# Optimization experiments

Hardware: AMD Instinct MI355X
Metric: run time of the kernel (lower is better)

Reference implementation:

```python
import jax, jax.numpy as jnp
import numpy as np

B = 32768          # batch (replay-buffer minibatch)
OBS, ACT = 17, 6   # HalfCheetah-style dims
IN = OBS + ACT
H = 256            # hidden width hard-coded in the module
N = 10             # num_q_nets


def setup_inputs() -> dict:
    key = jax.random.key(0)
    ks = jax.random.split(key, 8)
    # PyTorch Linear default init: U(-1/sqrt(fan_in), 1/sqrt(fan_in)); scale randn similarly.
    s1, s2, s3 = 1.0 / np.sqrt(IN), 1.0 / np.sqrt(H), 1.0 / np.sqrt(H)
    return {
        "state": jax.random.normal(ks[0], (B, OBS), dtype=jnp.float32),
        "action": jax.random.uniform(ks[1], (B, ACT), dtype=jnp.float32, minval=-1.0, maxval=1.0),
        "W1": jax.random.normal(ks[2], (N, IN, H), dtype=jnp.float32) * s1,
        "b1": jax.random.normal(ks[3], (N, H), dtype=jnp.float32) * s1,
        "W2": jax.random.normal(ks[4], (N, H, H), dtype=jnp.float32) * s2,
        "b2": jax.random.normal(ks[5], (N, H), dtype=jnp.float32) * s2,
        "W3": jax.random.normal(ks[6], (N, H, 1), dtype=jnp.float32) * s3,
        "b3": jax.random.normal(ks[7], (N, 1), dtype=jnp.float32) * s3,
    }


def reference(state, action, W1, b1, W2, b2, W3, b3):
    # x: [B, OBS+ACT]
    x = jnp.concatenate([state, action], axis=1)
    # batched-over-ensemble GEMMs; n=ensemble member, b=batch
    h1 = jax.nn.relu(jnp.einsum("bi,nih->nbh", x, W1) + b1[:, None, :])   # [N,B,H]
    h2 = jax.nn.relu(jnp.einsum("nbh,nho->nbo", h1, W2) + b2[:, None, :])  # [N,B,H]
    out = jnp.einsum("nbh,nho->nbo", h2, W3) + b3[:, None, :]              # [N,B,1]
    return out
```

## Files before the change

### kernel.cpp

```cpp
#include <hip/hip_runtime.h>
#include <hip/hip_bf16.h>


typedef __attribute__((ext_vector_type(8))) short bf16x8;
typedef __attribute__((ext_vector_type(4))) float f32x4;

#define B_TOTAL 32768
#define NQ 10
#define HDIM 256
#define BT 64

#define XP_ELEMS  (B_TOTAL * 32)
#define W1P_ELEMS (NQ * 16 * 64 * 8)
#define W2P_ELEMS (NQ * 8 * 16 * 64 * 8)

__device__ __forceinline__ unsigned short f2bf(float f) {
  unsigned int u = __float_as_uint(f);
  u = u + 0x7FFFu + ((u >> 16) & 1u);
  return (unsigned short)(u >> 16);
}

__device__ __forceinline__ unsigned int pk2bf(float a, float b) {
  union { __hip_bfloat162 h; unsigned int u; } cv;
  cv.h = __float22bfloat162_rn(make_float2(a, b));
  return cv.u;
}

__global__ void pack_all_kernel(const float* __restrict__ state,
                                const float* __restrict__ action,
                                const float* __restrict__ W1,
                                const float* __restrict__ W2,
                                unsigned short* __restrict__ xp,
                                unsigned short* __restrict__ w1p,
                                unsigned short* __restrict__ w2p) {
  int t = blockIdx.x * 256 + threadIdx.x;
  const int NX  = B_TOTAL * 4;
  const int NW1 = NQ * 16 * 64;
  if (t < NX) {
    int b = t >> 2, seg = t & 3;
    unsigned short v[8];
    if (seg < 2) {
      const float* sp = state + (size_t)b * 17 + seg * 8;
#pragma unroll
      for (int j = 0; j < 8; j++) v[j] = f2bf(sp[j]);
    } else if (seg == 2) {
      v[0] = f2bf(state[(size_t)b * 17 + 16]);
#pragma unroll
      for (int j = 0; j < 6; j++) v[1 + j] = f2bf(action[(size_t)b * 6 + j]);
      v[7] = 0;
    } else {
#pragma unroll
      for (int j = 0; j < 8; j++) v[j] = 0;
    }
    *(uint4*)&xp[(size_t)t * 8] = *(const uint4*)v;
  } else if (t < NX + NW1) {
    int u = t - NX;
    int lane = u & 63, mt = (u >> 6) & 15, n = u >> 10;
    int m = lane & 15, q = lane >> 4;
    int outc = mt * 16 + m;
    unsigned short v[8];
#pragma unroll
    for (int j = 0; j < 8; j++) {
      int k = q * 8 + j;
      v[j] = (k < 23) ? f2bf(W1[(n * 23 + k) * 256 + outc]) : (unsigned short)0;
    }
    *(uint4*)&w1p[(size_t)u * 8] = *(const uint4*)v;
  } else {
    int u = t - NX - NW1;
    int lane = u & 63, mt = (u >> 6) & 15, kt = (u >> 10) & 7, n = u >> 13;
    int m = lane & 15, q = lane >> 4;
    int outc = mt * 16 + m;
    unsigned short v[8];
#pragma unroll
    for (int j = 0; j < 8; j++) {
      int h = kt * 32 + q * 8 + j;
      v[j] = f2bf(W2[((size_t)(n * 256 + h)) * 256 + outc]);
    }
    *(uint4*)&w2p[(size_t)u * 8] = *(const uint4*)v;
  }
}

__global__ __launch_bounds__(256, 4) void fused_ensemble_kernel(
    const unsigned short* __restrict__ xp,
    const unsigned short* __restrict__ w1p,
    const float* __restrict__ b1,
    const unsigned short* __restrict__ w2p,
    const float* __restrict__ b2,
    const float* __restrict__ W3,
    const float* __restrict__ b3,
    float* __restrict__ out) {
  __shared__ __align__(16) unsigned short hs[32 * BT * 8];
  __shared__ float red[4 * 64];

  const int tid = threadIdx.x;
  const int lane = tid & 63;
  const int w = tid >> 6;
  const int m = lane & 15;
  const int q = lane >> 4;

  const int n = blockIdx.x >> 9;
  const int row0 = (blockIdx.x & 511) * BT;

  f32x4 acc[4][4];

  {
    bf16x8 af[4], bfr[4];
#pragma unroll
    for (int nt = 0; nt < 4; nt++) {
      int col = row0 + nt * 16 + m;
      bfr[nt] = *(const bf16x8*)(xp + (size_t)col * 32 + q * 8);
    }
#pragma unroll
    for (int mt = 0; mt < 4; mt++)
      af[mt] = *(const bf16x8*)(w1p + (((size_t)n * 16 + w * 4 + mt) * 64 + lane) * 8);
#pragma unroll
    for (int mt = 0; mt < 4; mt++) {
      float4 bv = *(const float4*)&b1[n * HDIM + (w * 4 + mt) * 16 + q * 4];
      f32x4 bi = (f32x4){bv.x, bv.y, bv.z, bv.w};
#pragma unroll
      for (int nt = 0; nt < 4; nt++) acc[mt][nt] = bi;
    }
    __builtin_amdgcn_s_setprio(1);
#pragma unroll
    for (int nt = 0; nt < 4; nt++)
#pragma unroll
      for (int mt = 0; mt < 4; mt++)
        acc[mt][nt] = __builtin_amdgcn_mfma_f32_16x16x32_bf16(af[mt], bfr[nt], acc[mt][nt], 0, 0, 0);
    __builtin_amdgcn_s_setprio(0);
  }

#pragma unroll
  for (int mt = 0; mt < 4; mt++) {
    int kq = w * 8 + mt * 2 + (q >> 1);
    int joff = (q & 1) * 4;
#pragma unroll
    for (int nt = 0; nt < 4; nt++) {
      int col = nt * 16 + m;
      f32x4 a = acc[mt][nt];
      uint2 wv;
      wv.x = pk2bf(fmaxf(a[0], 0.f), fmaxf(a[1], 0.f));
      wv.y = pk2bf(fmaxf(a[2], 0.f), fmaxf(a[3], 0.f));
      *(uint2*)&hs[((size_t)kq * BT + col) * 8 + joff] = wv;
    }
  }
  __syncthreads();

  {
    const unsigned short* w2n = w2p + (size_t)n * (8 * 16 * 64 * 8);
    bf16x8 acur[4], anxt[4];
#pragma unroll
    for (int mt = 0; mt < 4; mt++)
      acur[mt] = *(const bf16x8*)(w2n + (((size_t)w * 4 + mt) * 64 + lane) * 8);
#pragma unroll
    for (int mt = 0; mt < 4; mt++) {
      float4 bv = *(const float4*)&b2[n * HDIM + (w * 4 + mt) * 16 + q * 4];
      f32x4 bi = (f32x4){bv.x, bv.y, bv.z, bv.w};
#pragma unroll
      for (int nt = 0; nt < 4; nt++) acc[mt][nt] = bi;
    }
#pragma unroll
    for (int kt = 0; kt < 8; kt++) {
      if (kt < 7) {
#pragma unroll
        for (int mt = 0; mt < 4; mt++)
          anxt[mt] = *(const bf16x8*)(w2n + (((size_t)(kt + 1) * 16 + w * 4 + mt) * 64 + lane) * 8);
      }
      bf16x8 bfr[4];
#pragma unroll
      for (int nt = 0; nt < 4; nt++)
        bfr[nt] = *(const bf16x8*)&hs[(((size_t)kt * 4 + q) * BT + nt * 16 + m) * 8];
      __builtin_amdgcn_s_setprio(1);
#pragma unroll
      for (int nt = 0; nt < 4; nt++)
#pragma unroll
        for (int mt = 0; mt < 4; mt++)
          acc[mt][nt] = __builtin_amdgcn_mfma_f32_16x16x32_bf16(acur[mt], bfr[nt], acc[mt][nt], 0, 0, 0);
      __builtin_amdgcn_s_setprio(0);
#pragma unroll
      for (int mt = 0; mt < 4; mt++) acur[mt] = anxt[mt];
    }
  }

  {
    float4 w3v[4];
#pragma unroll
    for (int mt = 0; mt < 4; mt++)
      w3v[mt] = *(const float4*)&W3[n * HDIM + (w * 4 + mt) * 16 + q * 4];
    float p[4];
#pragma unroll
    for (int nt = 0; nt < 4; nt++) {
      float s = 0.f;
#pragma unroll
      for (int mt = 0; mt < 4; mt++) {
        f32x4 a = acc[mt][nt];
        float4 wv = w3v[mt];
        s = fmaf(fmaxf(a[0], 0.f), wv.x, s);
        s = fmaf(fmaxf(a[1], 0.f), wv.y, s);
        s = fmaf(fmaxf(a[2], 0.f), wv.z, s);
        s = fmaf(fmaxf(a[3], 0.f), wv.w, s);
      }
      s += __shfl_xor(s, 16, 64);
      s += __shfl_xor(s, 32, 64);
      p[nt] = s;
    }
    if (q == 0) {
#pragma unroll
      for (int nt = 0; nt < 4; nt++) red[w * 64 + nt * 16 + m] = p[nt];
    }
    __syncthreads();
    if (tid < BT) {
      float s = b3[n];
#pragma unroll
      for (int c = 0; c < 4; c++) s += red[c * 64 + tid];
      out[(size_t)n * B_TOTAL + row0 + tid] = s;
    }
  }
}

extern "C" void kernel_launch(void* const* d_in, const int* in_sizes, int n_in,
                              void* d_out, int out_size, void* d_ws, size_t ws_size,
                              hipStream_t stream) {
  const float* state  = (const float*)d_in[0];
  const float* action = (const float*)d_in[1];
  const float* W1 = (const float*)d_in[2];
  const float* b1 = (const float*)d_in[3];
  const float* W2 = (const float*)d_in[4];
  const float* b2 = (const float*)d_in[5];
  const float* W3 = (const float*)d_in[6];
  const float* b3 = (const float*)d_in[7];
  float* out = (float*)d_out;

  unsigned short* xp  = (unsigned short*)d_ws;
  unsigned short* w1p = (unsigned short*)((char*)d_ws + (size_t)XP_ELEMS * 2);
  unsigned short* w2p = (unsigned short*)((char*)d_ws + (size_t)(XP_ELEMS + W1P_ELEMS) * 2);

  pack_all_kernel<<<872, 256, 0, stream>>>(state, action, W1, W2, xp, w1p, w2p);
  fused_ensemble_kernel<<<NQ * (B_TOTAL / BT), 256, 0, stream>>>(
      xp, w1p, b1, w2p, b2, W3, b3, out);
}
```

Before: 119.7 us.

## Fold layer-1 bias into padded GEMM column and tidy layer-2/3 loops

Layer-1 bias goes into the unused 24th K slot of the packed weights, with a matching 1.0 in the packed input, so the MFMA applies it and the kernel no longer loads b1. The first W2 fragment and b2 loads are issued before the barrier, and W2 prefetch uses a ping-pong register array instead of copying. The final dot product uses packed 2-wide float math. Side effects: the bias is now rounded to bf16, and registers live across the barrier may raise pressure.

```diff
diff --git a/kernel.cpp b/kernel.cpp
--- a/kernel.cpp
+++ b/kernel.cpp
@@ -4,6 +4,7 @@
 
 typedef __attribute__((ext_vector_type(8))) short bf16x8;
 typedef __attribute__((ext_vector_type(4))) float f32x4;
+typedef __attribute__((ext_vector_type(2))) float f32x2;
 
 #define B_TOTAL 32768
 #define NQ 10
@@ -29,6 +30,7 @@
 __global__ void pack_all_kernel(const float* __restrict__ state,
                                 const float* __restrict__ action,
                                 const float* __restrict__ W1,
+                                const float* __restrict__ b1,
                                 const float* __restrict__ W2,
                                 unsigned short* __restrict__ xp,
                                 unsigned short* __restrict__ w1p,
@@ -47,7 +49,7 @@
       v[0] = f2bf(state[(size_t)b * 17 + 16]);
 #pragma unroll
       for (int j = 0; j < 6; j++) v[1 + j] = f2bf(action[(size_t)b * 6 + j]);
-      v[7] = 0;
+      v[7] = 0x3F80;
     } else {
 #pragma unroll
       for (int j = 0; j < 8; j++) v[j] = 0;
@@ -62,7 +64,8 @@
 #pragma unroll
     for (int j = 0; j < 8; j++) {
       int k = q * 8 + j;
-      v[j] = (k < 23) ? f2bf(W1[(n * 23 + k) * 256 + outc]) : (unsigned short)0;
+      v[j] = (k < 23) ? f2bf(W1[(n * 23 + k) * 256 + outc])
+           : (k == 23) ? f2bf(b1[n * 256 + outc]) : (unsigned short)0;
     }
     *(uint4*)&w1p[(size_t)u * 8] = *(const uint4*)v;
   } else {
@@ -83,7 +86,6 @@
 __global__ __launch_bounds__(256, 4) void fused_ensemble_kernel(
     const unsigned short* __restrict__ xp,
     const unsigned short* __restrict__ w1p,
-    const float* __restrict__ b1,
     const unsigned short* __restrict__ w2p,
     const float* __restrict__ b2,
     const float* __restrict__ W3,
@@ -104,7 +106,7 @@
   f32x4 acc[4][4];
 
   {
-    bf16x8 af[4], bfr[4];
+    bf16x8 af1[4], bfr[4];
 #pragma unroll
     for (int nt = 0; nt < 4; nt++) {
       int col = row0 + nt * 16 + m;
@@ -112,20 +114,17 @@
     }
 #pragma unroll
     for (int mt = 0; mt < 4; mt++)
-      af[mt] = *(const bf16x8*)(w1p + (((size_t)n * 16 + w * 4 + mt) * 64 + lane) * 8);
-#pragma unroll
-    for (int mt = 0; mt < 4; mt++) {
-      float4 bv = *(const float4*)&b1[n * HDIM + (w * 4 + mt) * 16 + q * 4];
-      f32x4 bi = (f32x4){bv.x, bv.y, bv.z, bv.w};
-#pragma unroll
-      for (int nt = 0; nt < 4; nt++) acc[mt][nt] = bi;
-    }
+      af1[mt] = *(const bf16x8*)(w1p + (((size_t)n * 16 + w * 4 + mt) * 64 + lane) * 8);
+#pragma unroll
+    for (int mt = 0; mt < 4; mt++)
+#pragma unroll
+      for (int nt = 0; nt < 4; nt++) acc[mt][nt] = (f32x4)0.0f;
     __builtin_amdgcn_s_setprio(1);
 #pragma unroll
     for (int nt = 0; nt < 4; nt++)
 #pragma unroll
       for (int mt = 0; mt < 4; mt++)
-        acc[mt][nt] = __builtin_amdgcn_mfma_f32_16x16x32_bf16(af[mt], bfr[nt], acc[mt][nt], 0, 0, 0);
+        acc[mt][nt] = __builtin_amdgcn_mfma_f32_16x16x32_bf16(af1[mt], bfr[nt], acc[mt][nt], 0, 0, 0);
     __builtin_amdgcn_s_setprio(0);
   }
 
@@ -136,34 +135,37 @@
 #pragma unroll
     for (int nt = 0; nt < 4; nt++) {
       int col = nt * 16 + m;
-      f32x4 a = acc[mt][nt];
+      f32x4 a = __builtin_elementwise_max(acc[mt][nt], (f32x4)0.0f);
       uint2 wv;
-      wv.x = pk2bf(fmaxf(a[0], 0.f), fmaxf(a[1], 0.f));
-      wv.y = pk2bf(fmaxf(a[2], 0.f), fmaxf(a[3], 0.f));
+      wv.x = pk2bf(a.x, a.y);
+      wv.y = pk2bf(a.z, a.w);
       *(uint2*)&hs[((size_t)kq * BT + col) * 8 + joff] = wv;
     }
   }
+
+  const unsigned short* w2n = w2p + (size_t)n * (8 * 16 * 64 * 8);
+  bf16x8 afb[2][4];
+#pragma unroll
+  for (int mt = 0; mt < 4; mt++)
+    afb[0][mt] = *(const bf16x8*)(w2n + (((size_t)w * 4 + mt) * 64 + lane) * 8);
+  f32x4 b2v[4];
+#pragma unroll
+  for (int mt = 0; mt < 4; mt++)
+    b2v[mt] = *(const f32x4*)&b2[n * HDIM + (w * 4 + mt) * 16 + q * 4];
   __syncthreads();
 
   {
-    const unsigned short* w2n = w2p + (size_t)n * (8 * 16 * 64 * 8);
-    bf16x8 acur[4], anxt[4];
-#pragma unroll
-    for (int mt = 0; mt < 4; mt++)
-      acur[mt] = *(const bf16x8*)(w2n + (((size_t)w * 4 + mt) * 64 + lane) * 8);
-#pragma unroll
-    for (int mt = 0; mt < 4; mt++) {
-      float4 bv = *(const float4*)&b2[n * HDIM + (w * 4 + mt) * 16 + q * 4];
-      f32x4 bi = (f32x4){bv.x, bv.y, bv.z, bv.w};
-#pragma unroll
-      for (int nt = 0; nt < 4; nt++) acc[mt][nt] = bi;
-    }
+#pragma unroll
+    for (int mt = 0; mt < 4; mt++)
+#pragma unroll
+      for (int nt = 0; nt < 4; nt++) acc[mt][nt] = b2v[mt];
 #pragma unroll
     for (int kt = 0; kt < 8; kt++) {
       if (kt < 7) {
 #pragma unroll
         for (int mt = 0; mt < 4; mt++)
-          anxt[mt] = *(const bf16x8*)(w2n + (((size_t)(kt + 1) * 16 + w * 4 + mt) * 64 + lane) * 8);
+          afb[(kt + 1) & 1][mt] =
+              *(const bf16x8*)(w2n + (((size_t)(kt + 1) * 16 + w * 4 + mt) * 64 + lane) * 8);
       }
       bf16x8 bfr[4];
 #pragma unroll
@@ -174,31 +176,28 @@
       for (int nt = 0; nt < 4; nt++)
 #pragma unroll
         for (int mt = 0; mt < 4; mt++)
-          acc[mt][nt] = __builtin_amdgcn_mfma_f32_16x16x32_bf16(acur[mt], bfr[nt], acc[mt][nt], 0, 0, 0);
+          acc[mt][nt] = __builtin_amdgcn_mfma_f32_16x16x32_bf16(afb[kt & 1][mt], bfr[nt],
+                                                               acc[mt][nt], 0, 0, 0);
       __builtin_amdgcn_s_setprio(0);
-#pragma unroll
-      for (int mt = 0; mt < 4; mt++) acur[mt] = anxt[mt];
     }
   }
 
   {
-    float4 w3v[4];
-#pragma unroll
-    for (int mt = 0; mt < 4; mt++)
-      w3v[mt] = *(const float4*)&W3[n * HDIM + (w * 4 + mt) * 16 + q * 4];
+    f32x4 w3v[4];
+#pragma unroll
+    for (int mt = 0; mt < 4; mt++)
+      w3v[mt] = *(const f32x4*)&W3[n * HDIM + (w * 4 + mt) * 16 + q * 4];
     float p[4];
 #pragma unroll
     for (int nt = 0; nt < 4; nt++) {
-      float s = 0.f;
+      f32x2 s2 = (f32x2)0.0f;
 #pragma unroll
       for (int mt = 0; mt < 4; mt++) {
-        f32x4 a = acc[mt][nt];
-        float4 wv = w3v[mt];
-        s = fmaf(fmaxf(a[0], 0.f), wv.x, s);
-        s = fmaf(fmaxf(a[1], 0.f), wv.y, s);
-        s = fmaf(fmaxf(a[2], 0.f), wv.z, s);
-        s = fmaf(fmaxf(a[3], 0.f), wv.w, s);
+        f32x4 a = __builtin_elementwise_max(acc[mt][nt], (f32x4)0.0f);
+        s2 += a.lo * w3v[mt].lo;
+        s2 += a.hi * w3v[mt].hi;
       }
+      float s = s2.x + s2.y;
       s += __shfl_xor(s, 16, 64);
       s += __shfl_xor(s, 32, 64);
       p[nt] = s;
@@ -234,7 +233,7 @@
   unsigned short* w1p = (unsigned short*)((char*)d_ws + (size_t)XP_ELEMS * 2);
   unsigned short* w2p = (unsigned short*)((char*)d_ws + (size_t)(XP_ELEMS + W1P_ELEMS) * 2);
 
-  pack_all_kernel<<<872, 256, 0, stream>>>(state, action, W1, W2, xp, w1p, w2p);
+  pack_all_kernel<<<872, 256, 0, stream>>>(state, action, W1, b1, W2, xp, w1p, w2p);
   fused_ensemble_kernel<<<NQ * (B_TOTAL / BT), 256, 0, stream>>>(
-      xp, w1p, b1, w2p, b2, W3, b3, out);
-}
+      xp, w1p, w2p, b2, W3, b3, out);
+}
```

Result: no change. 118.3 us (median of 2 runs) (-1.1%).
